# Kernel optimization log

Measured on AMD Instinct MI355X. Metric: run time of the kernel, lower is better.

The kernel has to match this reference:

```python
import jax, jax.numpy as jnp
import numpy as np
import math

B, N, M = 4, 2048, 2048
DIM_Q = DIM_K = DIM_V = 1024
H = 16

def setup_inputs() -> dict:
    key = jax.random.key(0)
    ks = jax.random.split(key, 10)
    s = 0.02
    return {
        "Q": jax.random.normal(ks[0], (B, N, DIM_Q), jnp.float32),
        "K": jax.random.normal(ks[1], (B, M, DIM_K), jnp.float32),
        "Wq": jax.random.normal(ks[2], (DIM_V, DIM_Q), jnp.float32) * s,
        "bq": jax.random.normal(ks[3], (DIM_V,), jnp.float32) * s,
        "Wk": jax.random.normal(ks[4], (DIM_V, DIM_K), jnp.float32) * s,
        "bk": jax.random.normal(ks[5], (DIM_V,), jnp.float32) * s,
        "Wv": jax.random.normal(ks[6], (DIM_V, DIM_K), jnp.float32) * s,
        "bv": jax.random.normal(ks[7], (DIM_V,), jnp.float32) * s,
        "Wo": jax.random.normal(ks[8], (DIM_V, DIM_V), jnp.float32) * s,
        "bo": jax.random.normal(ks[9], (DIM_V,), jnp.float32) * s,
    }

def reference(Q, K, Wq, bq, Wk, bk, Wv, bv, Wo, bo):
    d = DIM_V // H  # head dim
    Qp = Q @ Wq.T + bq            # [B,N,DIM_V]
    Kp = K @ Wk.T + bk            # [B,M,DIM_V]
    Vp = K @ Wv.T + bv            # [B,M,DIM_V]
    # split heads: [B,T,H,d] -> [B,H,T,d]
    Qh = Qp.reshape(B, N, H, d).transpose(0, 2, 1, 3)
    Kh = Kp.reshape(B, M, H, d).transpose(0, 2, 1, 3)
    Vh = Vp.reshape(B, M, H, d).transpose(0, 2, 1, 3)
    # NOTE: original scales by sqrt(dim_V), not sqrt(head_dim)
    scores = jnp.einsum('bhnd,bhmd->bhnm', Qh, Kh) / math.sqrt(DIM_V)
    A = jax.nn.softmax(scores, axis=-1)
    Oh = Qh + jnp.einsum('bhnm,bhmd->bhnd', A, Vh)   # residual with projected Q
    O = Oh.transpose(0, 2, 1, 3).reshape(B, N, DIM_V)
    O = O + jax.nn.relu(O @ Wo.T + bo)
    return O
```

## Files before the change

kernel.cpp:

```cpp
#include <hip/hip_runtime.h>
#include <cstddef>
#include <cstdint>


typedef unsigned short ushort_t;
typedef __attribute__((ext_vector_type(8))) short bf16x8;
typedef __attribute__((ext_vector_type(4))) float floatx4;
typedef __attribute__((ext_vector_type(8))) unsigned short us8;
typedef __attribute__((ext_vector_type(4))) unsigned short us4;

__device__ __forceinline__ ushort_t f2bf(float x) {
  union { float f; unsigned u; } v; v.f = x;
  unsigned r = v.u + 0x7FFFu + ((v.u >> 16) & 1u);
  return (ushort_t)(r >> 16);
}
__device__ __forceinline__ float bf2f(ushort_t x) {
  union { unsigned u; float f; } v; v.u = ((unsigned)x) << 16;
  return v.f;
}
__device__ __forceinline__ unsigned pk2(float a, float b) {
  union { float f; unsigned u; } x, y; x.f = a; y.f = b;
  return __builtin_amdgcn_perm(y.u + 0x8000u, x.u + 0x8000u, 0x07060302u);
}
__device__ __forceinline__ floatx4 mfma16(bf16x8 a, bf16x8 b, floatx4 c) {
  return __builtin_amdgcn_mfma_f32_16x16x32_bf16(a, b, c, 0, 0, 0);
}
__device__ __forceinline__ void gld_lds16(const void* g, void* l) {
  __builtin_amdgcn_global_load_lds(
      (const __attribute__((address_space(1))) unsigned int*)g,
      (__attribute__((address_space(3))) unsigned int*)l, 16, 0, 0);
}

__global__ void cvt4(const float* __restrict__ i0, const float* __restrict__ i1,
                     const float* __restrict__ i2, const float* __restrict__ i3,
                     ushort_t* __restrict__ o0, ushort_t* __restrict__ o1,
                     ushort_t* __restrict__ o2, ushort_t* __restrict__ o3, int n8) {
  int z = blockIdx.z;
  const float* in = z == 0 ? i0 : z == 1 ? i1 : z == 2 ? i2 : i3;
  ushort_t* out = z == 0 ? o0 : z == 1 ? o1 : z == 2 ? o2 : o3;
  int i = blockIdx.x * 256 + threadIdx.x;
  if (i < n8) {
    const float4* p = (const float4*)in + (size_t)i * 2;
    float4 a = p[0], b = p[1];
    uint4 o;
    o.x = pk2(a.x, a.y); o.y = pk2(a.z, a.w);
    o.z = pk2(b.x, b.y); o.w = pk2(b.z, b.w);
    *((uint4*)out + i) = o;
  }
}

__global__ __launch_bounds__(256, 2)
void gemm_qkv(const ushort_t* __restrict__ Qb, const ushort_t* __restrict__ Kb,
              const ushort_t* __restrict__ Wqb, const ushort_t* __restrict__ Wkb,
              const ushort_t* __restrict__ Wvb,
              const float* __restrict__ bq, const float* __restrict__ bk,
              const float* __restrict__ bv,
              ushort_t* __restrict__ Qp, ushort_t* __restrict__ Kp,
              ushort_t* __restrict__ Vt)
{
  const int Kd = 1024, Nn = 1024;
  const int z = blockIdx.z;
  const ushort_t* Ab = (z == 0) ? Qb : Kb;
  const ushort_t* Bw = (z == 0) ? Wqb : (z == 1) ? Wkb : Wvb;
  const float* bias  = (z == 0) ? bq : (z == 1) ? bk : bv;

  __shared__ __align__(16) ushort_t As[128][32];
  __shared__ __align__(16) ushort_t Bs[128][32];
  const int tid = threadIdx.x;
  const int lane = tid & 63, wave = tid >> 6;
  const int wm = (wave >> 1) * 64, wn = (wave & 1) * 64;
  const int rq = lane & 15, kg = lane >> 4;
  const int row0 = blockIdx.y * 128, col0 = blockIdx.x * 128;

  const int st_row = (lane >> 2);
  const int st_cs  = (lane & 3) ^ ((lane >> 3) & 3);
  const int rd_ch  = ((rq >> 1) & 3);

  floatx4 acc[4][4];
#pragma unroll
  for (int i = 0; i < 4; ++i)
#pragma unroll
    for (int j = 0; j < 4; ++j) acc[i][j] = (floatx4){0.f, 0.f, 0.f, 0.f};

  for (int k0 = 0; k0 < Kd; k0 += 32) {
    __syncthreads();
#pragma unroll
    for (int r = 0; r < 2; ++r) {
      int i = wave * 2 + r;
      int row = i * 16 + st_row;
      gld_lds16(Ab + (size_t)(row0 + row) * Kd + k0 + st_cs * 8, (ushort_t*)As + i * 512);
      gld_lds16(Bw + (size_t)(col0 + row) * Kd + k0 + st_cs * 8, (ushort_t*)Bs + i * 512);
    }
    __syncthreads();
    bf16x8 af[4], bfr[4];
#pragma unroll
    for (int mi = 0; mi < 4; ++mi)
      af[mi] = *(const bf16x8*)&As[wm + mi*16 + rq][(kg ^ rd_ch) * 8];
#pragma unroll
    for (int ni = 0; ni < 4; ++ni)
      bfr[ni] = *(const bf16x8*)&Bs[wn + ni*16 + rq][(kg ^ rd_ch) * 8];
#pragma unroll
    for (int mi = 0; mi < 4; ++mi)
#pragma unroll
      for (int ni = 0; ni < 4; ++ni)
        acc[mi][ni] = mfma16(af[mi], bfr[ni], acc[mi][ni]);
  }

  float bv4[4];
#pragma unroll
  for (int ni = 0; ni < 4; ++ni) bv4[ni] = bias[col0 + wn + ni*16 + rq];

  if (z < 2) {
    ushort_t* Cb = (z == 0) ? Qp : Kp;
#pragma unroll
    for (int mi = 0; mi < 4; ++mi)
#pragma unroll
      for (int ni = 0; ni < 4; ++ni)
#pragma unroll
        for (int rr = 0; rr < 4; ++rr) {
          int row = row0 + wm + mi*16 + kg*4 + rr;
          int col = col0 + wn + ni*16 + rq;
          Cb[(size_t)row * Nn + col] = f2bf(acc[mi][ni][rr] + bv4[ni]);
        }
  } else {
#pragma unroll
    for (int mi = 0; mi < 4; ++mi)
#pragma unroll
      for (int ni = 0; ni < 4; ++ni) {
        int col = col0 + wn + ni*16 + rq;
        int r0  = row0 + wm + mi*16 + kg*4;
        us4 o = { f2bf(acc[mi][ni][0] + bv4[ni]), f2bf(acc[mi][ni][1] + bv4[ni]),
                  f2bf(acc[mi][ni][2] + bv4[ni]), f2bf(acc[mi][ni][3] + bv4[ni]) };
        *(us4*)(Vt + (size_t)col * 8192 + r0) = o;
      }
  }
}

__global__ __launch_bounds__(256, 2)
void gemm_out(const ushort_t* __restrict__ Ob, const ushort_t* __restrict__ Bw,
              const float* __restrict__ bias, float* __restrict__ Out)
{
  const int Kd = 1024, Nn = 1024;
  __shared__ __align__(16) ushort_t As[128][32];
  __shared__ __align__(16) ushort_t Bs[128][32];
  const int tid = threadIdx.x;
  const int lane = tid & 63, wave = tid >> 6;
  const int wm = (wave >> 1) * 64, wn = (wave & 1) * 64;
  const int rq = lane & 15, kg = lane >> 4;
  const int row0 = blockIdx.y * 128, col0 = blockIdx.x * 128;

  const int st_row = (lane >> 2);
  const int st_cs  = (lane & 3) ^ ((lane >> 3) & 3);
  const int rd_ch  = ((rq >> 1) & 3);

  floatx4 acc[4][4];
#pragma unroll
  for (int i = 0; i < 4; ++i)
#pragma unroll
    for (int j = 0; j < 4; ++j) acc[i][j] = (floatx4){0.f, 0.f, 0.f, 0.f};

  for (int k0 = 0; k0 < Kd; k0 += 32) {
    __syncthreads();
#pragma unroll
    for (int r = 0; r < 2; ++r) {
      int i = wave * 2 + r;
      int row = i * 16 + st_row;
      gld_lds16(Ob + (size_t)(row0 + row) * Kd + k0 + st_cs * 8, (ushort_t*)As + i * 512);
      gld_lds16(Bw + (size_t)(col0 + row) * Kd + k0 + st_cs * 8, (ushort_t*)Bs + i * 512);
    }
    __syncthreads();
    bf16x8 af[4], bfr[4];
#pragma unroll
    for (int mi = 0; mi < 4; ++mi)
      af[mi] = *(const bf16x8*)&As[wm + mi*16 + rq][(kg ^ rd_ch) * 8];
#pragma unroll
    for (int ni = 0; ni < 4; ++ni)
      bfr[ni] = *(const bf16x8*)&Bs[wn + ni*16 + rq][(kg ^ rd_ch) * 8];
#pragma unroll
    for (int mi = 0; mi < 4; ++mi)
#pragma unroll
      for (int ni = 0; ni < 4; ++ni)
        acc[mi][ni] = mfma16(af[mi], bfr[ni], acc[mi][ni]);
  }

  float bv4[4];
#pragma unroll
  for (int ni = 0; ni < 4; ++ni) bv4[ni] = bias[col0 + wn + ni*16 + rq];
#pragma unroll
  for (int mi = 0; mi < 4; ++mi)
#pragma unroll
    for (int ni = 0; ni < 4; ++ni)
#pragma unroll
      for (int rr = 0; rr < 4; ++rr) {
        int row = row0 + wm + mi*16 + kg*4 + rr;
        int col = col0 + wn + ni*16 + rq;
        size_t idx = (size_t)row * Nn + col;
        float pre = acc[mi][ni][rr] + bv4[ni];
        Out[idx] = bf2f(Ob[idx]) + (pre > 0.f ? pre : 0.f);
      }
}

__global__ __launch_bounds__(256, 2)
void attn_kernel(const ushort_t* __restrict__ Qp,
                 const ushort_t* __restrict__ Kp,
                 const ushort_t* __restrict__ Vt,
                 ushort_t* __restrict__ Ob)
{
  const float sc2 = 0.045084439f;
  const int qt = blockIdx.x;
  const int bh = blockIdx.y;
  const int b = bh >> 4, h = bh & 15;
  const int q0 = qt * 128;

  __shared__ __align__(16) ushort_t Ks[128][64];
  __shared__ __align__(16) ushort_t Vs[64][128];
  __shared__ __align__(16) ushort_t Ps[128][128];
  __shared__ float reds[2][128];

  const int tid = threadIdx.x, lane = tid & 63, wave = tid >> 6;
  const int whalf = wave >> 1;
  const int wsec  = wave & 1;
  const int rq = lane & 15, kg = lane >> 4;

  const size_t qkbase = (size_t)(b * 2048) * 1024 + h * 64;

#pragma unroll
  for (int r = 0; r < 4; ++r) {
    int i = wave * 4 + r;
    int row = i * 8 + (lane >> 3);
    int cs = (lane & 7) ^ (row & 7);
    gld_lds16(Qp + qkbase + (size_t)(q0 + row) * 1024 + cs * 8, (ushort_t*)Ks + i * 512);
  }
  __syncthreads();

  bf16x8 aq[4][2];
#pragma unroll
  for (int ni = 0; ni < 4; ++ni)
#pragma unroll
    for (int kq = 0; kq < 2; ++kq) {
      int row = wsec*64 + ni*16 + rq;
      int ch = (kq*4 + kg) ^ (rq & 7);
      bf16x8 t = *(const bf16x8*)&Ks[row][ch * 8];
#pragma unroll
      for (int e = 0; e < 8; ++e)
        t[e] = (short)f2bf(bf2f((ushort_t)t[e]) * sc2);
      aq[ni][kq] = t;
    }

  floatx4 oacc[4][2];
  float l_st[4];
#pragma unroll
  for (int mi = 0; mi < 4; ++mi) {
    oacc[mi][0] = (floatx4){0.f,0.f,0.f,0.f};
    oacc[mi][1] = (floatx4){0.f,0.f,0.f,0.f};
  }
#pragma unroll
  for (int ni = 0; ni < 4; ++ni) l_st[ni] = 0.f;

  for (int kt = 0; kt < 16; ++kt) {
    const int kv0 = kt * 128;
    __syncthreads();
#pragma unroll
    for (int r = 0; r < 4; ++r) {
      int i = wave * 4 + r;
      int row = i * 8 + (lane >> 3);
      int cs = (lane & 7) ^ (row & 7);
      gld_lds16(Kp + qkbase + (size_t)(kv0 + row) * 1024 + cs * 8, (ushort_t*)Ks + i * 512);
    }
#pragma unroll
    for (int r = 0; r < 4; ++r) {
      int i = wave * 4 + r;
      int dv = i * 4 + (lane >> 4);
      int cs = (lane & 15) ^ (dv & 7);
      gld_lds16(Vt + (size_t)(h*64 + dv) * 8192 + b * 2048 + kv0 + cs * 8,
                (ushort_t*)Vs + i * 512);
    }
    __syncthreads();

    floatx4 s[4][4];
#pragma unroll
    for (int mi = 0; mi < 4; ++mi)
#pragma unroll
      for (int ni = 0; ni < 4; ++ni) s[mi][ni] = (floatx4){0.f,0.f,0.f,0.f};
#pragma unroll
    for (int kq = 0; kq < 2; ++kq) {
      bf16x8 ak[4];
#pragma unroll
      for (int mi = 0; mi < 4; ++mi) {
        int row = whalf*64 + mi*16 + rq;
        int ch = (kq*4 + kg) ^ (rq & 7);
        ak[mi] = *(const bf16x8*)&Ks[row][ch * 8];
      }
#pragma unroll
      for (int mi = 0; mi < 4; ++mi)
#pragma unroll
        for (int ni = 0; ni < 4; ++ni)
          s[mi][ni] = mfma16(ak[mi], aq[ni][kq], s[mi][ni]);
    }

#pragma unroll
    for (int mi = 0; mi < 4; ++mi)
#pragma unroll
      for (int ni = 0; ni < 4; ++ni)
#pragma unroll
        for (int rr = 0; rr < 4; ++rr)
          s[mi][ni][rr] = __builtin_amdgcn_exp2f(s[mi][ni][rr]);
#pragma unroll
    for (int ni = 0; ni < 4; ++ni) {
      float t = 0.f;
#pragma unroll
      for (int mi = 0; mi < 4; ++mi)
        t += (s[mi][ni][0] + s[mi][ni][1]) + (s[mi][ni][2] + s[mi][ni][3]);
      l_st[ni] += t;
    }

#pragma unroll
    for (int mi = 0; mi < 4; ++mi)
#pragma unroll
      for (int ni = 0; ni < 4; ++ni) {
        int q = wsec*64 + ni*16 + rq;
        int chunk = (whalf*8 + mi*2 + (kg >> 1)) ^ rq;
        int colu = chunk*8 + (kg & 1)*4;
        uint2 w;
        w.x = pk2(s[mi][ni][0], s[mi][ni][1]);
        w.y = pk2(s[mi][ni][2], s[mi][ni][3]);
        *(uint2*)&Ps[q][colu] = w;
      }
    __syncthreads();

#pragma unroll
    for (int kp = 0; kp < 4; ++kp) {
      bf16x8 pf[4], vf[2];
#pragma unroll
      for (int mi = 0; mi < 4; ++mi) {
        int row = whalf*64 + mi*16 + rq;
        int slot = (kp*4 + kg) ^ rq;
        pf[mi] = *(const bf16x8*)&Ps[row][slot * 8];
      }
#pragma unroll
      for (int n2 = 0; n2 < 2; ++n2) {
        int dv = wsec*32 + n2*16 + rq;
        int ch = (kp*4 + kg) ^ (rq & 7);
        vf[n2] = *(const bf16x8*)&Vs[dv][ch * 8];
      }
#pragma unroll
      for (int mi = 0; mi < 4; ++mi)
#pragma unroll
        for (int n2 = 0; n2 < 2; ++n2)
          oacc[mi][n2] = mfma16(pf[mi], vf[n2], oacc[mi][n2]);
    }
  }

#pragma unroll
  for (int ni = 0; ni < 4; ++ni) {
    l_st[ni] += __shfl_xor(l_st[ni], 16, 64);
    l_st[ni] += __shfl_xor(l_st[ni], 32, 64);
  }
  if (lane < 16) {
#pragma unroll
    for (int ni = 0; ni < 4; ++ni)
      reds[whalf][wsec*64 + ni*16 + rq] = l_st[ni];
  }
  __syncthreads();

#pragma unroll
  for (int mi = 0; mi < 4; ++mi)
#pragma unroll
    for (int rr = 0; rr < 4; ++rr) {
      int row = whalf*64 + mi*16 + kg*4 + rr;
      float linv = 1.0f / (reds[0][row] + reds[1][row]);
#pragma unroll
      for (int n2 = 0; n2 < 2; ++n2) {
        int col = wsec*32 + n2*16 + rq;
        size_t idx = qkbase + (size_t)(q0 + row) * 1024 + col;
        float ov = oacc[mi][n2][rr] * linv + bf2f(Qp[idx]);
        Ob[idx] = f2bf(ov);
      }
    }
}

extern "C" void kernel_launch(void* const* d_in, const int* in_sizes, int n_in,
                              void* d_out, int out_size, void* d_ws, size_t ws_size,
                              hipStream_t stream)
{
  const float* Q  = (const float*)d_in[0];
  const float* K  = (const float*)d_in[1];
  const float* Wq = (const float*)d_in[2];
  const float* bq = (const float*)d_in[3];
  const float* Wk = (const float*)d_in[4];
  const float* bk = (const float*)d_in[5];
  const float* Wv = (const float*)d_in[6];
  const float* bv = (const float*)d_in[7];
  const float* Wo = (const float*)d_in[8];
  const float* bo = (const float*)d_in[9];
  float* Out = (float*)d_out;

  ushort_t* ws = (ushort_t*)d_ws;
  const size_t E = (size_t)8192 * 1024;
  const size_t WSZ = (size_t)1024 * 1024;
  ushort_t* Qb  = ws;
  ushort_t* Kb  = ws + E;
  ushort_t* Qp  = ws + 2*E;
  ushort_t* Kp  = ws + 3*E;
  ushort_t* Vt  = ws + 4*E;
  ushort_t* Wqb = ws + 5*E;
  ushort_t* Wkb = ws + 5*E + WSZ;
  ushort_t* Wvb = ws + 5*E + 2*WSZ;
  ushort_t* Wob = ws + 5*E + 3*WSZ;
  ushort_t* Ob  = Qb;

  cvt4<<<dim3(4096, 1, 2), 256, 0, stream>>>(Q, K, K, K, Qb, Kb, Kb, Kb, 1048576);
  cvt4<<<dim3(512, 1, 4), 256, 0, stream>>>(Wq, Wk, Wv, Wo, Wqb, Wkb, Wvb, Wob, 131072);

  dim3 blk(256);
  gemm_qkv<<<dim3(8, 64, 3), blk, 0, stream>>>(Qb, Kb, Wqb, Wkb, Wvb,
                                               bq, bk, bv, Qp, Kp, Vt);
  attn_kernel<<<dim3(16, 64), blk, 0, stream>>>(Qp, Kp, Vt, Ob);
  gemm_out<<<dim3(8, 64), blk, 0, stream>>>(Ob, Wob, bo, Out);
}
```

Measured before the change: 343.2 us.

## Deepen GEMM K-tiles to 64, alias K/V shared buffers in attention, raise occupancy

Both projection GEMMs now stage 64-wide K slices with a new 8-chunk XOR swizzle, which halves the number of barrier-separated iterations. The attention kernel shares one LDS buffer between K and V: it loads K, computes scores, syncs, then loads V into the same space while exp and P writes run. The lower LDS footprint, together with launch bounds raised from 2 to 3 blocks per CU, is meant to fit more blocks per CU. The cost is an extra barrier in attention, V loads that can no longer overlap the QK MFMAs, and tighter register limits that may cause spills.

```diff
diff --git a/kernel.cpp b/kernel.cpp
--- a/kernel.cpp
+++ b/kernel.cpp
@@ -49,7 +49,7 @@
   }
 }
 
-__global__ __launch_bounds__(256, 2)
+__global__ __launch_bounds__(256, 3)
 void gemm_qkv(const ushort_t* __restrict__ Qb, const ushort_t* __restrict__ Kb,
               const ushort_t* __restrict__ Wqb, const ushort_t* __restrict__ Wkb,
               const ushort_t* __restrict__ Wvb,
@@ -64,17 +64,16 @@
   const ushort_t* Bw = (z == 0) ? Wqb : (z == 1) ? Wkb : Wvb;
   const float* bias  = (z == 0) ? bq : (z == 1) ? bk : bv;
 
-  __shared__ __align__(16) ushort_t As[128][32];
-  __shared__ __align__(16) ushort_t Bs[128][32];
+  __shared__ __align__(16) ushort_t As[128][64];
+  __shared__ __align__(16) ushort_t Bs[128][64];
   const int tid = threadIdx.x;
   const int lane = tid & 63, wave = tid >> 6;
   const int wm = (wave >> 1) * 64, wn = (wave & 1) * 64;
   const int rq = lane & 15, kg = lane >> 4;
   const int row0 = blockIdx.y * 128, col0 = blockIdx.x * 128;
 
-  const int st_row = (lane >> 2);
-  const int st_cs  = (lane & 3) ^ ((lane >> 3) & 3);
-  const int rd_ch  = ((rq >> 1) & 3);
+  const int st_sub = lane >> 3;
+  const int st_cs  = (lane & 7) ^ st_sub;
 
   floatx4 acc[4][4];
 #pragma unroll
@@ -82,28 +81,31 @@
 #pragma unroll
     for (int j = 0; j < 4; ++j) acc[i][j] = (floatx4){0.f, 0.f, 0.f, 0.f};
 
-  for (int k0 = 0; k0 < Kd; k0 += 32) {
-    __syncthreads();
-#pragma unroll
-    for (int r = 0; r < 2; ++r) {
-      int i = wave * 2 + r;
-      int row = i * 16 + st_row;
+  for (int k0 = 0; k0 < Kd; k0 += 64) {
+    __syncthreads();
+#pragma unroll
+    for (int r = 0; r < 4; ++r) {
+      int i = wave * 4 + r;
+      int row = i * 8 + st_sub;
       gld_lds16(Ab + (size_t)(row0 + row) * Kd + k0 + st_cs * 8, (ushort_t*)As + i * 512);
       gld_lds16(Bw + (size_t)(col0 + row) * Kd + k0 + st_cs * 8, (ushort_t*)Bs + i * 512);
     }
     __syncthreads();
-    bf16x8 af[4], bfr[4];
-#pragma unroll
-    for (int mi = 0; mi < 4; ++mi)
-      af[mi] = *(const bf16x8*)&As[wm + mi*16 + rq][(kg ^ rd_ch) * 8];
-#pragma unroll
-    for (int ni = 0; ni < 4; ++ni)
-      bfr[ni] = *(const bf16x8*)&Bs[wn + ni*16 + rq][(kg ^ rd_ch) * 8];
-#pragma unroll
-    for (int mi = 0; mi < 4; ++mi)
+#pragma unroll
+    for (int kq = 0; kq < 2; ++kq) {
+      bf16x8 af[4], bfr[4];
+#pragma unroll
+      for (int mi = 0; mi < 4; ++mi)
+        af[mi] = *(const bf16x8*)&As[wm + mi*16 + rq][((kq*4 + kg) ^ (rq & 7)) * 8];
 #pragma unroll
       for (int ni = 0; ni < 4; ++ni)
-        acc[mi][ni] = mfma16(af[mi], bfr[ni], acc[mi][ni]);
+        bfr[ni] = *(const bf16x8*)&Bs[wn + ni*16 + rq][((kq*4 + kg) ^ (rq & 7)) * 8];
+#pragma unroll
+      for (int mi = 0; mi < 4; ++mi)
+#pragma unroll
+        for (int ni = 0; ni < 4; ++ni)
+          acc[mi][ni] = mfma16(af[mi], bfr[ni], acc[mi][ni]);
+    }
   }
 
   float bv4[4];
@@ -136,22 +138,21 @@
   }
 }
 
-__global__ __launch_bounds__(256, 2)
+__global__ __launch_bounds__(256, 3)
 void gemm_out(const ushort_t* __restrict__ Ob, const ushort_t* __restrict__ Bw,
               const float* __restrict__ bias, float* __restrict__ Out)
 {
   const int Kd = 1024, Nn = 1024;
-  __shared__ __align__(16) ushort_t As[128][32];
-  __shared__ __align__(16) ushort_t Bs[128][32];
+  __shared__ __align__(16) ushort_t As[128][64];
+  __shared__ __align__(16) ushort_t Bs[128][64];
   const int tid = threadIdx.x;
   const int lane = tid & 63, wave = tid >> 6;
   const int wm = (wave >> 1) * 64, wn = (wave & 1) * 64;
   const int rq = lane & 15, kg = lane >> 4;
   const int row0 = blockIdx.y * 128, col0 = blockIdx.x * 128;
 
-  const int st_row = (lane >> 2);
-  const int st_cs  = (lane & 3) ^ ((lane >> 3) & 3);
-  const int rd_ch  = ((rq >> 1) & 3);
+  const int st_sub = lane >> 3;
+  const int st_cs  = (lane & 7) ^ st_sub;
 
   floatx4 acc[4][4];
 #pragma unroll
@@ -159,28 +160,31 @@
 #pragma unroll
     for (int j = 0; j < 4; ++j) acc[i][j] = (floatx4){0.f, 0.f, 0.f, 0.f};
 
-  for (int k0 = 0; k0 < Kd; k0 += 32) {
-    __syncthreads();
-#pragma unroll
-    for (int r = 0; r < 2; ++r) {
-      int i = wave * 2 + r;
-      int row = i * 16 + st_row;
+  for (int k0 = 0; k0 < Kd; k0 += 64) {
+    __syncthreads();
+#pragma unroll
+    for (int r = 0; r < 4; ++r) {
+      int i = wave * 4 + r;
+      int row = i * 8 + st_sub;
       gld_lds16(Ob + (size_t)(row0 + row) * Kd + k0 + st_cs * 8, (ushort_t*)As + i * 512);
       gld_lds16(Bw + (size_t)(col0 + row) * Kd + k0 + st_cs * 8, (ushort_t*)Bs + i * 512);
     }
     __syncthreads();
-    bf16x8 af[4], bfr[4];
-#pragma unroll
-    for (int mi = 0; mi < 4; ++mi)
-      af[mi] = *(const bf16x8*)&As[wm + mi*16 + rq][(kg ^ rd_ch) * 8];
-#pragma unroll
-    for (int ni = 0; ni < 4; ++ni)
-      bfr[ni] = *(const bf16x8*)&Bs[wn + ni*16 + rq][(kg ^ rd_ch) * 8];
-#pragma unroll
-    for (int mi = 0; mi < 4; ++mi)
+#pragma unroll
+    for (int kq = 0; kq < 2; ++kq) {
+      bf16x8 af[4], bfr[4];
+#pragma unroll
+      for (int mi = 0; mi < 4; ++mi)
+        af[mi] = *(const bf16x8*)&As[wm + mi*16 + rq][((kq*4 + kg) ^ (rq & 7)) * 8];
 #pragma unroll
       for (int ni = 0; ni < 4; ++ni)
-        acc[mi][ni] = mfma16(af[mi], bfr[ni], acc[mi][ni]);
+        bfr[ni] = *(const bf16x8*)&Bs[wn + ni*16 + rq][((kq*4 + kg) ^ (rq & 7)) * 8];
+#pragma unroll
+      for (int mi = 0; mi < 4; ++mi)
+#pragma unroll
+        for (int ni = 0; ni < 4; ++ni)
+          acc[mi][ni] = mfma16(af[mi], bfr[ni], acc[mi][ni]);
+    }
   }
 
   float bv4[4];
@@ -200,7 +204,7 @@
       }
 }
 
-__global__ __launch_bounds__(256, 2)
+__global__ __launch_bounds__(256, 3)
 void attn_kernel(const ushort_t* __restrict__ Qp,
                  const ushort_t* __restrict__ Kp,
                  const ushort_t* __restrict__ Vt,
@@ -212,8 +216,7 @@
   const int b = bh >> 4, h = bh & 15;
   const int q0 = qt * 128;
 
-  __shared__ __align__(16) ushort_t Ks[128][64];
-  __shared__ __align__(16) ushort_t Vs[64][128];
+  __shared__ __align__(16) ushort_t KVs[8192];
   __shared__ __align__(16) ushort_t Ps[128][128];
   __shared__ float reds[2][128];
 
@@ -228,8 +231,8 @@
   for (int r = 0; r < 4; ++r) {
     int i = wave * 4 + r;
     int row = i * 8 + (lane >> 3);
-    int cs = (lane & 7) ^ (row & 7);
-    gld_lds16(Qp + qkbase + (size_t)(q0 + row) * 1024 + cs * 8, (ushort_t*)Ks + i * 512);
+    int cs = (lane & 7) ^ (lane >> 3);
+    gld_lds16(Qp + qkbase + (size_t)(q0 + row) * 1024 + cs * 8, KVs + i * 512);
   }
   __syncthreads();
 
@@ -240,7 +243,7 @@
     for (int kq = 0; kq < 2; ++kq) {
       int row = wsec*64 + ni*16 + rq;
       int ch = (kq*4 + kg) ^ (rq & 7);
-      bf16x8 t = *(const bf16x8*)&Ks[row][ch * 8];
+      bf16x8 t = *(const bf16x8*)&KVs[row * 64 + ch * 8];
 #pragma unroll
       for (int e = 0; e < 8; ++e)
         t[e] = (short)f2bf(bf2f((ushort_t)t[e]) * sc2);
@@ -264,38 +267,40 @@
     for (int r = 0; r < 4; ++r) {
       int i = wave * 4 + r;
       int row = i * 8 + (lane >> 3);
-      int cs = (lane & 7) ^ (row & 7);
-      gld_lds16(Kp + qkbase + (size_t)(kv0 + row) * 1024 + cs * 8, (ushort_t*)Ks + i * 512);
-    }
+      int cs = (lane & 7) ^ (lane >> 3);
+      gld_lds16(Kp + qkbase + (size_t)(kv0 + row) * 1024 + cs * 8, KVs + i * 512);
+    }
+    __syncthreads();
+
+    floatx4 s[4][4];
+#pragma unroll
+    for (int mi = 0; mi < 4; ++mi)
+#pragma unroll
+      for (int ni = 0; ni < 4; ++ni) s[mi][ni] = (floatx4){0.f,0.f,0.f,0.f};
+#pragma unroll
+    for (int kq = 0; kq < 2; ++kq) {
+      bf16x8 ak[4];
+#pragma unroll
+      for (int mi = 0; mi < 4; ++mi) {
+        int row = whalf*64 + mi*16 + rq;
+        int ch = (kq*4 + kg) ^ (rq & 7);
+        ak[mi] = *(const bf16x8*)&KVs[row * 64 + ch * 8];
+      }
+#pragma unroll
+      for (int mi = 0; mi < 4; ++mi)
+#pragma unroll
+        for (int ni = 0; ni < 4; ++ni)
+          s[mi][ni] = mfma16(ak[mi], aq[ni][kq], s[mi][ni]);
+    }
+    __syncthreads();
+
 #pragma unroll
     for (int r = 0; r < 4; ++r) {
       int i = wave * 4 + r;
       int dv = i * 4 + (lane >> 4);
       int cs = (lane & 15) ^ (dv & 7);
       gld_lds16(Vt + (size_t)(h*64 + dv) * 8192 + b * 2048 + kv0 + cs * 8,
-                (ushort_t*)Vs + i * 512);
-    }
-    __syncthreads();
-
-    floatx4 s[4][4];
-#pragma unroll
-    for (int mi = 0; mi < 4; ++mi)
-#pragma unroll
-      for (int ni = 0; ni < 4; ++ni) s[mi][ni] = (floatx4){0.f,0.f,0.f,0.f};
-#pragma unroll
-    for (int kq = 0; kq < 2; ++kq) {
-      bf16x8 ak[4];
-#pragma unroll
-      for (int mi = 0; mi < 4; ++mi) {
-        int row = whalf*64 + mi*16 + rq;
-        int ch = (kq*4 + kg) ^ (rq & 7);
-        ak[mi] = *(const bf16x8*)&Ks[row][ch * 8];
-      }
-#pragma unroll
-      for (int mi = 0; mi < 4; ++mi)
-#pragma unroll
-        for (int ni = 0; ni < 4; ++ni)
-          s[mi][ni] = mfma16(ak[mi], aq[ni][kq], s[mi][ni]);
+                KVs + i * 512);
     }
 
 #pragma unroll
@@ -313,7 +318,6 @@
         t += (s[mi][ni][0] + s[mi][ni][1]) + (s[mi][ni][2] + s[mi][ni][3]);
       l_st[ni] += t;
     }
-
 #pragma unroll
     for (int mi = 0; mi < 4; ++mi)
 #pragma unroll
@@ -341,7 +345,7 @@
       for (int n2 = 0; n2 < 2; ++n2) {
         int dv = wsec*32 + n2*16 + rq;
         int ch = (kp*4 + kg) ^ (rq & 7);
-        vf[n2] = *(const bf16x8*)&Vs[dv][ch * 8];
+        vf[n2] = *(const bf16x8*)&KVs[dv * 128 + ch * 8];
       }
 #pragma unroll
       for (int mi = 0; mi < 4; ++mi)
```

Measured after the change: 388.8 us. +13.3%, slower.
